# Performance work log

Measured on AMD Instinct MI355X. Metric: run time of the kernel, lower is better.

The kernel has to match this reference:

```python
import jax, jax.numpy as jnp
import numpy as np

TOP_K = 8  # config['n_experts_per_token']


def setup_inputs() -> dict:
    key = jax.random.key(0)
    k1, k2 = jax.random.split(key)
    d_hidden, n_experts, n_tokens = 4096, 64, 32768
    x = jax.random.normal(k1, (n_tokens, d_hidden), dtype=jnp.float32)
    # nn.Linear weight, shape [num_experts, d_hidden], kaiming-ish scale
    W_g = jax.random.normal(k2, (n_experts, d_hidden), dtype=jnp.float32) / np.sqrt(d_hidden)
    return {"x": x, "W_g": W_g}


def reference(x, W_g):
    # logits = x @ W_g^T : [n_tokens, n_experts]
    logits = jnp.einsum('td,ed->te', x, W_g)
    scores = jax.nn.softmax(logits, axis=-1)
    # torch.topk(sorted=False) returns the same value/index set; lax.top_k is sorted
    vals, idx = jax.lax.top_k(scores, TOP_K)
    return vals, idx
```

## Files before the change

kernel.cpp:

```cpp
#include <hip/hip_runtime.h>
#include <hip/hip_fp16.h>


typedef _Float16 half8 __attribute__((ext_vector_type(8)));
typedef float floatx4 __attribute__((ext_vector_type(4)));

constexpr int D = 4096;
constexpr int NE = 64;
constexpr int MBLK = 64;
constexpr int BK = 64;
constexpr int KCHUNKS = D / BK;

constexpr size_t WPACK_OFF  = 1u << 18;
constexpr size_t WPACK_HALF = (size_t)KCHUNKS * NE * BK;

__device__ __forceinline__ void split8s(float4 p, float4 q, float sc, half8& h, half8& l) {
    float f[8] = {p.x, p.y, p.z, p.w, q.x, q.y, q.z, q.w};
#pragma unroll
    for (int i = 0; i < 8; ++i) {
        float v = f[i] * sc;
        _Float16 hi = (_Float16)v;
        h[i] = hi;
        l[i] = (_Float16)(v - (float)hi);
    }
}

__device__ __forceinline__ void async16(const _Float16* g, _Float16* lds) {
    __builtin_amdgcn_global_load_lds(
        (__attribute__((address_space(1))) uint32_t*)g,
        (__attribute__((address_space(3))) uint32_t*)lds, 16, 0, 0);
}

__global__ __launch_bounds__(256) void moe_pack_w(
    const float* __restrict__ wg, _Float16* __restrict__ whp, _Float16* __restrict__ wlp)
{
    const int kc = (int)blockIdx.x;
    const int tid = (int)threadIdx.x;
#pragma unroll
    for (int r = 0; r < 2; ++r) {
        const int s = tid + r * 256;
        const int e = s >> 3, k8 = s & 7;
        const float* src = wg + (size_t)e * D + kc * BK + k8 * 8;
        float4 a = *(const float4*)src;
        float4 b = *(const float4*)(src + 4);
        half8 h, l;
        split8s(a, b, 64.0f, h, l);
        const int off = (((e >> 4) * 2 + (k8 >> 2)) * 64 + (k8 & 3) * 16 + (e & 15)) * 8;
        *(half8*)(whp + (size_t)kc * 4096 + off) = h;
        *(half8*)(wlp + (size_t)kc * 4096 + off) = l;
    }
}

__global__ __launch_bounds__(256, 2) void moe_gate_kernel(
    const float* __restrict__ x,
    const _Float16* __restrict__ whp, const _Float16* __restrict__ wlp,
    float* __restrict__ out_vals, float* __restrict__ out_idx,
    int* __restrict__ flag_ws, int cap)
{
    __shared__ alignas(16) _Float16 WhB[2 * NE * BK];
    __shared__ alignas(16) _Float16 WlB[2 * NE * BK];

    const int tid  = (int)threadIdx.x;
    const int lane = tid & 63;
    const int wv   = tid >> 6;
    const int tb   = (int)blockIdx.x * MBLK;

    const float* xp = x + (size_t)(tb + wv * 16 + (lane & 15)) * D + (lane >> 4) * 8;

    const int wgo = wv * 1024 + lane * 8;
    const int wlo = wv * 1024;

    floatx4 acc[4] = {{0,0,0,0},{0,0,0,0},{0,0,0,0},{0,0,0,0}};

    async16(whp + wgo,       WhB + wlo);
    async16(whp + wgo + 512, WhB + wlo + 512);
    async16(wlp + wgo,       WlB + wlo);
    async16(wlp + wgo + 512, WlB + wlo + 512);
    float4 A0 = *(const float4*)(xp);
    float4 A1 = *(const float4*)(xp + 4);
    float4 A2 = *(const float4*)(xp + 32);
    float4 A3 = *(const float4*)(xp + 36);
    float4 B0, B1, B2, B3;
    asm volatile("s_waitcnt vmcnt(0)" ::: "memory");
    __syncthreads();

    auto body = [&](int kc, float4& C0, float4& C1, float4& C2, float4& C3,
                    float4& N0, float4& N1, float4& N2, float4& N3) {
        if (kc + 1 < KCHUNKS) {
            const int nb = (kc + 1) & 1;
            const _Float16* gh = whp + (size_t)(kc + 1) * 4096 + wgo;
            const _Float16* gl = wlp + (size_t)(kc + 1) * 4096 + wgo;
            async16(gh,       WhB + nb * 4096 + wlo);
            async16(gh + 512, WhB + nb * 4096 + wlo + 512);
            async16(gl,       WlB + nb * 4096 + wlo);
            async16(gl + 512, WlB + nb * 4096 + wlo + 512);
            const float* xn = xp + (kc + 1) * 64;
            N0 = *(const float4*)(xn);
            N1 = *(const float4*)(xn + 4);
            N2 = *(const float4*)(xn + 32);
            N3 = *(const float4*)(xn + 36);
        }
        half8 ah0, al0, ah1, al1;
        split8s(C0, C1, 1.0f, ah0, al0);
        split8s(C2, C3, 1.0f, ah1, al1);
        const _Float16* wh = WhB + (kc & 1) * 4096;
        const _Float16* wl = WlB + (kc & 1) * 4096;
#pragma unroll
        for (int nt = 0; nt < 4; ++nt) {
            const half8 bh = *(const half8*)(wh + ((nt * 2 + 0) * 64 + lane) * 8);
            const half8 bl = *(const half8*)(wl + ((nt * 2 + 0) * 64 + lane) * 8);
            acc[nt] = __builtin_amdgcn_mfma_f32_16x16x32_f16(ah0, bh, acc[nt], 0, 0, 0);
            acc[nt] = __builtin_amdgcn_mfma_f32_16x16x32_f16(al0, bh, acc[nt], 0, 0, 0);
            acc[nt] = __builtin_amdgcn_mfma_f32_16x16x32_f16(ah0, bl, acc[nt], 0, 0, 0);
        }
#pragma unroll
        for (int nt = 0; nt < 4; ++nt) {
            const half8 bh = *(const half8*)(wh + ((nt * 2 + 1) * 64 + lane) * 8);
            const half8 bl = *(const half8*)(wl + ((nt * 2 + 1) * 64 + lane) * 8);
            acc[nt] = __builtin_amdgcn_mfma_f32_16x16x32_f16(ah1, bh, acc[nt], 0, 0, 0);
            acc[nt] = __builtin_amdgcn_mfma_f32_16x16x32_f16(al1, bh, acc[nt], 0, 0, 0);
            acc[nt] = __builtin_amdgcn_mfma_f32_16x16x32_f16(ah1, bl, acc[nt], 0, 0, 0);
        }
        asm volatile("s_waitcnt vmcnt(0)" ::: "memory");
        __syncthreads();
    };

    for (int kc = 0; kc < KCHUNKS; kc += 2) {
        body(kc,     A0, A1, A2, A3, B0, B1, B2, B3);
        body(kc + 1, B0, B1, B2, B3, A0, A1, A2, A3);
    }

    const int g = lane >> 4, c = lane & 15;
    const float inv64 = 0.015625f;
#pragma unroll
    for (int r = 0; r < 4; ++r) {
        float s[4];
#pragma unroll
        for (int nt = 0; nt < 4; ++nt) s[nt] = acc[nt][r] * inv64;
        float m = fmaxf(fmaxf(s[0], s[1]), fmaxf(s[2], s[3]));
#pragma unroll
        for (int off = 1; off < 16; off <<= 1) m = fmaxf(m, __shfl_xor(m, off));
        float p[4]; float t = 0.0f;
#pragma unroll
        for (int nt = 0; nt < 4; ++nt) { p[nt] = expf(s[nt] - m); t += p[nt]; }
#pragma unroll
        for (int off = 1; off < 16; off <<= 1) t += __shfl_xor(t, off);
        const float inv = 1.0f / t;
#pragma unroll
        for (int nt = 0; nt < 4; ++nt) p[nt] *= inv;

        const int tok = tb + wv * 16 + g * 4 + r;
        float prev = 0.0f;
        bool flagged = false;
#pragma unroll
        for (int i = 0; i < 9; ++i) {
            float bv = p[0]; int bn = 0;
            if (p[1] > bv) { bv = p[1]; bn = 1; }
            if (p[2] > bv) { bv = p[2]; bn = 2; }
            if (p[3] > bv) { bv = p[3]; bn = 3; }
            int be = bn * 16 + c;
#pragma unroll
            for (int off = 1; off < 16; off <<= 1) {
                float ov = __shfl_xor(bv, off);
                int   oe = __shfl_xor(be, off);
                if (ov > bv || (ov == bv && oe < be)) { bv = ov; be = oe; }
            }
            if (i > 0 && (prev - bv) < prev * 5e-5f) flagged = true;
            prev = bv;
            if (i < 8 && c == i) {
                out_vals[(size_t)tok * 8 + i] = bv;
                out_idx [(size_t)tok * 8 + i] = (float)be;
            }
            if (c == (be & 15)) p[be >> 4] = -1.0f;
        }
        if (flagged && c == 0 && cap > 0) {
            int pos = atomicAdd(flag_ws, 1);
            if (pos < cap) flag_ws[4 + pos] = tok;
        }
    }
}

__global__ __launch_bounds__(256) void moe_refine_kernel(
    const float* __restrict__ x, const float* __restrict__ wg,
    float* __restrict__ out_vals, float* __restrict__ out_idx,
    const int* __restrict__ flag_ws, int cap)
{
    const int count = min(flag_ws[0], cap);
    const int* list = flag_ws + 4;
    __shared__ double part[256];
    for (int it = (int)blockIdx.x; it < count; it += (int)gridDim.x) {
        const int tok = list[it];
        const int e = (int)threadIdx.x & 63, ch = (int)threadIdx.x >> 6;
        const float4* xr = (const float4*)(x + (size_t)tok * D + ch * 1024);
        const float4* wr = (const float4*)(wg + (size_t)e * D + ch * 1024);
        double s0 = 0, s1 = 0, s2 = 0, s3 = 0;
#pragma unroll 4
        for (int k = 0; k < 256; ++k) {
            float4 a = xr[k], b = wr[k];
            s0 += (double)a.x * (double)b.x; s1 += (double)a.y * (double)b.y;
            s2 += (double)a.z * (double)b.z; s3 += (double)a.w * (double)b.w;
        }
        part[threadIdx.x] = (s0 + s1) + (s2 + s3);
        __syncthreads();
        if (threadIdx.x < 64) {
            double l = part[e] + part[e + 64] + part[e + 128] + part[e + 192];
            double m = l;
#pragma unroll
            for (int off = 1; off < 64; off <<= 1) m = fmax(m, __shfl_xor(m, off));
            double p = exp(l - m), Z = p;
#pragma unroll
            for (int off = 1; off < 64; off <<= 1) Z += __shfl_xor(Z, off);
            double key = l;
            for (int i = 0; i < 8; ++i) {
                double bk = key; int bi = e; double bp = p;
#pragma unroll
                for (int off = 1; off < 64; off <<= 1) {
                    double ok = __shfl_xor(bk, off);
                    int    oi = __shfl_xor(bi, off);
                    double op = __shfl_xor(bp, off);
                    if (ok > bk || (ok == bk && oi < bi)) { bk = ok; bi = oi; bp = op; }
                }
                if (e == i) {
                    out_vals[(size_t)tok * 8 + i] = (float)(bp / Z);
                    out_idx [(size_t)tok * 8 + i] = (float)bi;
                }
                if (e == bi) key = -1.0e300;
            }
        }
        __syncthreads();
    }
}

extern "C" void kernel_launch(void* const* d_in, const int* in_sizes, int n_in,
                              void* d_out, int out_size, void* d_ws, size_t ws_size,
                              hipStream_t stream) {
    const float* x  = (const float*)d_in[0];
    const float* wg = (const float*)d_in[1];
    const int n_tokens = in_sizes[0] / D;
    float* out_vals = (float*)d_out;
    float* out_idx  = out_vals + (size_t)n_tokens * 8;
    _Float16* whp = (_Float16*)((char*)d_ws + WPACK_OFF);
    _Float16* wlp = whp + WPACK_HALF;
    int cap = 0;
    if (ws_size > 32) {
        size_t c = (ws_size - 32) / sizeof(int);
        cap = (int)(c > 32768 ? 32768 : c);
    }
    hipMemsetAsync(d_ws, 0, 16, stream);
    hipLaunchKernelGGL(moe_pack_w, dim3(KCHUNKS), dim3(256), 0, stream, wg, whp, wlp);
    const int grid = n_tokens / MBLK;
    hipLaunchKernelGGL(moe_gate_kernel, dim3(grid), dim3(256), 0, stream,
                       x, whp, wlp, out_vals, out_idx, (int*)d_ws, cap);
    hipLaunchKernelGGL(moe_refine_kernel, dim3(256), dim3(256), 0, stream,
                       x, wg, out_vals, out_idx, (const int*)d_ws, cap);
}
```

Before: 787.0 us.

## Deepen weight LDS pipeline to four buffers with prefetch distance two

The gate kernel now uses four LDS slots for the packed weight chunks and issues async loads two chunks ahead. It waits with a partial vmcnt instead of draining all loads, and uses a raw s_barrier, so global latency can overlap with the MFMA work. The workspace memset is folded into the pack kernel, and the pack kernel now runs one element per thread on 128 blocks. LDS use doubles, which may limit occupancy. The vmcnt counting depends on the order loads are issued, which the compiler could break.

```diff
diff --git a/kernel.cpp b/kernel.cpp
--- a/kernel.cpp
+++ b/kernel.cpp
@@ -31,24 +31,24 @@
         (__attribute__((address_space(3))) uint32_t*)lds, 16, 0, 0);
 }
 
+#define MEMFENCE() asm volatile("" ::: "memory")
+
 __global__ __launch_bounds__(256) void moe_pack_w(
-    const float* __restrict__ wg, _Float16* __restrict__ whp, _Float16* __restrict__ wlp)
+    const float* __restrict__ wg, _Float16* __restrict__ whp,
+    _Float16* __restrict__ wlp, int* __restrict__ flag_ws)
 {
-    const int kc = (int)blockIdx.x;
-    const int tid = (int)threadIdx.x;
-#pragma unroll
-    for (int r = 0; r < 2; ++r) {
-        const int s = tid + r * 256;
-        const int e = s >> 3, k8 = s & 7;
-        const float* src = wg + (size_t)e * D + kc * BK + k8 * 8;
-        float4 a = *(const float4*)src;
-        float4 b = *(const float4*)(src + 4);
-        half8 h, l;
-        split8s(a, b, 64.0f, h, l);
-        const int off = (((e >> 4) * 2 + (k8 >> 2)) * 64 + (k8 & 3) * 16 + (e & 15)) * 8;
-        *(half8*)(whp + (size_t)kc * 4096 + off) = h;
-        *(half8*)(wlp + (size_t)kc * 4096 + off) = l;
-    }
+    if (blockIdx.x == 0 && threadIdx.x < 4) flag_ws[threadIdx.x] = 0;
+    const int s  = (int)blockIdx.x * 256 + (int)threadIdx.x;
+    const int kc = s >> 9, sc = s & 511;
+    const int e  = sc >> 3, k8 = sc & 7;
+    const float* src = wg + (size_t)e * D + kc * BK + k8 * 8;
+    float4 a = *(const float4*)src;
+    float4 b = *(const float4*)(src + 4);
+    half8 h, l;
+    split8s(a, b, 64.0f, h, l);
+    const int off = (((e >> 4) * 2 + (k8 >> 2)) * 64 + (k8 & 3) * 16 + (e & 15)) * 8;
+    *(half8*)(whp + (size_t)kc * 4096 + off) = h;
+    *(half8*)(wlp + (size_t)kc * 4096 + off) = l;
 }
 
 __global__ __launch_bounds__(256, 2) void moe_gate_kernel(
@@ -57,8 +57,8 @@
     float* __restrict__ out_vals, float* __restrict__ out_idx,
     int* __restrict__ flag_ws, int cap)
 {
-    __shared__ alignas(16) _Float16 WhB[2 * NE * BK];
-    __shared__ alignas(16) _Float16 WlB[2 * NE * BK];
+    __shared__ alignas(16) _Float16 WhB[4 * NE * BK];
+    __shared__ alignas(16) _Float16 WlB[4 * NE * BK];
 
     const int tid  = (int)threadIdx.x;
     const int lane = tid & 63;
@@ -76,35 +76,49 @@
     async16(whp + wgo + 512, WhB + wlo + 512);
     async16(wlp + wgo,       WlB + wlo);
     async16(wlp + wgo + 512, WlB + wlo + 512);
+    MEMFENCE();
     float4 A0 = *(const float4*)(xp);
     float4 A1 = *(const float4*)(xp + 4);
     float4 A2 = *(const float4*)(xp + 32);
     float4 A3 = *(const float4*)(xp + 36);
+    MEMFENCE();
+    {
+        const _Float16* gh = whp + 4096 + wgo;
+        const _Float16* gl = wlp + 4096 + wgo;
+        async16(gh,       WhB + 4096 + wlo);
+        async16(gh + 512, WhB + 4096 + wlo + 512);
+        async16(gl,       WlB + 4096 + wlo);
+        async16(gl + 512, WlB + 4096 + wlo + 512);
+    }
     float4 B0, B1, B2, B3;
-    asm volatile("s_waitcnt vmcnt(0)" ::: "memory");
-    __syncthreads();
+    asm volatile("s_waitcnt vmcnt(4)" ::: "memory");
+    __builtin_amdgcn_s_barrier();
+    MEMFENCE();
 
     auto body = [&](int kc, float4& C0, float4& C1, float4& C2, float4& C3,
                     float4& N0, float4& N1, float4& N2, float4& N3) {
         if (kc + 1 < KCHUNKS) {
-            const int nb = (kc + 1) & 1;
-            const _Float16* gh = whp + (size_t)(kc + 1) * 4096 + wgo;
-            const _Float16* gl = wlp + (size_t)(kc + 1) * 4096 + wgo;
-            async16(gh,       WhB + nb * 4096 + wlo);
-            async16(gh + 512, WhB + nb * 4096 + wlo + 512);
-            async16(gl,       WlB + nb * 4096 + wlo);
-            async16(gl + 512, WlB + nb * 4096 + wlo + 512);
             const float* xn = xp + (kc + 1) * 64;
             N0 = *(const float4*)(xn);
             N1 = *(const float4*)(xn + 4);
             N2 = *(const float4*)(xn + 32);
             N3 = *(const float4*)(xn + 36);
         }
+        MEMFENCE();
+        if (kc + 2 < KCHUNKS) {
+            const _Float16* gh = whp + (size_t)(kc + 2) * 4096 + wgo;
+            const _Float16* gl = wlp + (size_t)(kc + 2) * 4096 + wgo;
+            const int sl = ((kc + 2) & 3) * 4096;
+            async16(gh,       WhB + sl + wlo);
+            async16(gh + 512, WhB + sl + wlo + 512);
+            async16(gl,       WlB + sl + wlo);
+            async16(gl + 512, WlB + sl + wlo + 512);
+        }
         half8 ah0, al0, ah1, al1;
         split8s(C0, C1, 1.0f, ah0, al0);
         split8s(C2, C3, 1.0f, ah1, al1);
-        const _Float16* wh = WhB + (kc & 1) * 4096;
-        const _Float16* wl = WlB + (kc & 1) * 4096;
+        const _Float16* wh = WhB + (kc & 3) * 4096;
+        const _Float16* wl = WlB + (kc & 3) * 4096;
 #pragma unroll
         for (int nt = 0; nt < 4; ++nt) {
             const half8 bh = *(const half8*)(wh + ((nt * 2 + 0) * 64 + lane) * 8);
@@ -121,8 +135,12 @@
             acc[nt] = __builtin_amdgcn_mfma_f32_16x16x32_f16(al1, bh, acc[nt], 0, 0, 0);
             acc[nt] = __builtin_amdgcn_mfma_f32_16x16x32_f16(ah1, bl, acc[nt], 0, 0, 0);
         }
-        asm volatile("s_waitcnt vmcnt(0)" ::: "memory");
-        __syncthreads();
+        if (kc + 1 < KCHUNKS) {
+            if (kc + 2 < KCHUNKS) asm volatile("s_waitcnt vmcnt(4)" ::: "memory");
+            else                  asm volatile("s_waitcnt vmcnt(0)" ::: "memory");
+            __builtin_amdgcn_s_barrier();
+            MEMFENCE();
+        }
     };
 
     for (int kc = 0; kc < KCHUNKS; kc += 2) {
@@ -246,8 +264,8 @@
         size_t c = (ws_size - 32) / sizeof(int);
         cap = (int)(c > 32768 ? 32768 : c);
     }
-    hipMemsetAsync(d_ws, 0, 16, stream);
-    hipLaunchKernelGGL(moe_pack_w, dim3(KCHUNKS), dim3(256), 0, stream, wg, whp, wlp);
+    hipLaunchKernelGGL(moe_pack_w, dim3(128), dim3(256), 0, stream,
+                       wg, whp, wlp, (int*)d_ws);
     const int grid = n_tokens / MBLK;
     hipLaunchKernelGGL(moe_gate_kernel, dim3(grid), dim3(256), 0, stream,
                        x, whp, wlp, out_vals, out_idx, (int*)d_ws, cap);
```

After: 795.2 us. No clear change (+1.0%).
